# Kernel tuning notes

Hardware: AMD Instinct MI355X
Metric: run time of the kernel (lower is better)

Reference implementation:

```python
import jax, jax.numpy as jnp
import numpy as np

A_CONST = -50.0  # self.a in FNNnew


def _fnn_all(t, w1, b1, w2, b2):
    # Evaluate the 4 tiny FNNs (f, f_prime, g, g_prime) at once.
    # t: (L,); w1: (4,5,1); b1: (4,5); w2: (4,1,5); b2: (4,1) -> (4, L)
    z = jnp.tanh(jnp.einsum('l,kh->klh', t, w1[:, :, 0]) + b1[:, None, :])  # (4,L,5)
    out = jnp.einsum('klh,kh->kl', z, w2[:, 0, :]) + b2  # (4,L)
    return out * jnp.exp(A_CONST * t)[None, :]


def setup_inputs() -> dict:
    key = jax.random.key(0)
    ks = jax.random.split(key, 5)
    bs, d, T = 32, 8, 8192
    return {
        'x_data': jax.random.normal(ks[0], (bs, d, T), dtype=jnp.float32),
        'fnn_w1': jax.random.normal(ks[1], (4, 5, 1), dtype=jnp.float32) * 0.1,
        'fnn_b1': jax.random.normal(ks[2], (4, 5), dtype=jnp.float32) * 0.1,
        'fnn_w2': jax.random.normal(ks[3], (4, 1, 5), dtype=jnp.float32) * 0.1,
        'fnn_b2': jax.random.normal(ks[4], (4, 1), dtype=jnp.float32) * 0.1,
        'words': 8,
    }


def reference(x_data, fnn_w1, fnn_b1, fnn_w2, fnn_b2, words):
    bs, d, T = x_data.shape
    N = 3 * T + 1  # padded FFT length
    t = jnp.arange(T + 1, dtype=jnp.float32)

    arrs = _fnn_all(t, fnn_w1, fnn_b1, fnn_w2, fnn_b2)  # (4, T+1)
    f_arr = arrs[0][::-1]      # f, flipped
    fp_arr = arrs[1][::-1]     # f_prime, flipped
    g_arr = arrs[2]            # g
    gp_arr = arrs[3]           # g_prime

    pad1 = lambda a: jnp.pad(a, (T, T))  # (T+1,) -> (N,)
    Hf = jnp.fft.fft(pad1(f_arr))
    Hfp = jnp.fft.fft(pad1(fp_arr))
    Hg = jnp.fft.fft(pad1(g_arr))
    Hgp = jnp.fft.fft(pad1(gp_arr))
    Hones = jnp.fft.fft(pad1(jnp.ones(T + 1, jnp.float32)))

    # ISS low-rank arrays for all words at once (word k uses channels k%d, (k+1)%d)
    k = jnp.arange(words)
    dx1 = x_data[:, k % d, :]        # (bs, words, T)
    dx2 = x_data[:, (k + 1) % d, :]  # (bs, words, T)
    c1 = jnp.cumsum(dx1, -1)
    c2 = jnp.cumsum(dx2, -1)
    c1_prev = jnp.concatenate([jnp.zeros_like(c1[..., :1]), c1[..., :-1]], -1)
    pre0 = lambda a: jnp.concatenate([jnp.zeros_like(a[..., :1]), a], -1)  # -> length T+1
    iss_sum = pre0(jnp.cumsum(dx2 * c1_prev, -1))   # iterated sum <12>
    cs_d1 = pre0(c1)                                 # consecutive sum, level 1
    cs_d2 = pre0(c2)                                 # consecutive sum, level 2
    iss_d1 = pre0(jnp.cumsum(dx1 * dx2, -1))        # diagonal term

    pad3 = lambda a: jnp.pad(a, ((0, 0), (0, 0), (T, T)))
    F = lambda a: jnp.fft.fft(pad3(a), axis=-1)  # (bs, words, N) complex
    ISSf, C1f, C2f, D1f = F(iss_sum), F(cs_d1), F(cs_d2), F(iss_d1)

    conv = lambda Ha, Hb: jnp.fft.ifft(Ha * Hb, axis=-1)

    AA = conv(Hf, ISSf)
    AB = jnp.fft.ifft(Hg * Hones)       # (N,)
    BA = conv(Hfp, ISSf)
    BB = jnp.fft.ifft(Hgp * Hones)
    CA = conv(Hf, C1f)
    CB = conv(Hg, C2f)
    DA = conv(Hfp, C1f)
    DB = conv(Hgp, C2f)
    EA = jnp.fft.ifft(Hf * Hones)       # (N,)
    EB = conv(Hg, D1f)
    FA = jnp.fft.ifft(Hfp * Hones)      # (N,)
    FB = conv(Hgp, D1f)

    out = 0.5 * (AA * AB[None, None, :] + BA * BB[None, None, :]
                 + CA * CB + DA * DB
                 + EA[None, None, :] * EB + FA[None, None, :] * FB)
    return out.real[..., 2 * T:]  # (bs, words, T+1)
```

## Files before the change

kernel.cpp:

```cpp
#include <hip/hip_runtime.h>


constexpr int T  = 8192;
constexpr int BS = 32;
constexpr int D  = 8;
constexpr int W  = 8;
constexpr int L  = 3;

__global__ __launch_bounds__(256)
void pdn_kernel(const float* __restrict__ x,
                const float* __restrict__ w1,
                const float* __restrict__ b1,
                const float* __restrict__ w2,
                const float* __restrict__ b2,
                float* __restrict__ out)
{
    const int row = blockIdx.x;
    const int bb  = row >> 3;
    const int wd  = row & 7;
    const int tid = threadIdx.x;
    const float* dx1 = x + ((size_t)bb * D + wd) * T;
    const float* dx2 = x + ((size_t)bb * D + ((wd + 1) & 7)) * T;
    const size_t base = (size_t)row * (T + 1);
    float* orow = out + base;

    float s2 = 0.f, p = 0.f;
    const float4* v1 = (const float4*)dx1;
    const float4* v2 = (const float4*)dx2;
    #pragma unroll 4
    for (int t = tid; t < T / 4; t += 256) {
        float4 a = v1[t], c = v2[t];
        s2 += (c.x + c.y) + (c.z + c.w);
        p  += a.x * c.x + a.y * c.y + a.z * c.z + a.w * c.w;
    }

    const int align = (int)((4 - (base & 3)) & 3);
    if (tid < align) orow[tid] = 0.f;
    const int nvec = (T + 1 - align) >> 2;
    const int rem  = (T + 1 - align) - (nvec << 2);
    float4* ov = (float4*)(orow + align);
    const float4 z4 = make_float4(0.f, 0.f, 0.f, 0.f);
    #pragma unroll 4
    for (int i = tid; i < nvec; i += 256) ov[i] = z4;
    if (tid < rem) orow[align + (nvec << 2) + tid] = 0.f;

    for (int off = 32; off > 0; off >>= 1) {
        s2 += __shfl_down(s2, off);
        p  += __shfl_down(p,  off);
    }
    __shared__ float sh[2][4];
    __shared__ float term[4 * L * 5];
    const int wave = tid >> 6, lane = tid & 63;
    if (lane == 0) { sh[0][wave] = s2; sh[1][wave] = p; }

    if (tid < 4 * L * 5) {
        const int k = tid / (L * 5);
        const int r = tid % (L * 5);
        const int l = r / 5, h = r % 5;
        term[tid] = tanhf((float)l * w1[k * 5 + h] + b1[k * 5 + h]) * w2[k * 5 + h];
    }
    __syncthreads();

    if (tid != 0) return;

    const float s2tot = sh[0][0] + sh[0][1] + sh[0][2] + sh[0][3];
    const float ptot  = sh[1][0] + sh[1][1] + sh[1][2] + sh[1][3];

    const float e[L] = {1.0f, expf(-50.0f), expf(-100.0f)};
    float F[4][L];
    for (int k = 0; k < 4; ++k)
        for (int l = 0; l < L; ++l) {
            float acc = b2[k];
            for (int h = 0; h < 5; ++h) acc += term[(k * L + l) * 5 + h];
            F[k][l] = acc * e[l];
        }

    float S1[L], Q[L];
    S1[0] = 0.f; Q[0] = 0.f;
    for (int j = 1; j < L; ++j) {
        S1[j] = S1[j - 1] + dx1[j - 1];
        Q[j]  = Q[j - 1] + dx2[j - 1] * S1[j - 1];
    }
    float S2v[2 * L - 1], Pv[2 * L - 1];
    S2v[0] = s2tot; Pv[0] = ptot;
    for (int i = 1; i < 2 * L - 1; ++i) {
        S2v[i] = S2v[i - 1] - dx2[T - i];
        Pv[i]  = Pv[i - 1]  - dx1[T - i] * dx2[T - i];
    }
    float Gsum = 0.f, GPsum = 0.f;
    for (int l = 0; l < L; ++l) { Gsum += F[2][l]; GPsum += F[3][l]; }

    for (int m = 0; m < L; ++m) {
        float AA = 0, BA = 0, CA = 0, DA = 0, EA = 0, FA = 0;
        for (int l = m; l < L; ++l) {
            const float q = Q[l - m], s1 = S1[l - m];
            AA += F[0][l] * q;   BA += F[1][l] * q;
            CA += F[0][l] * s1;  DA += F[1][l] * s1;
            EA += F[0][l];       FA += F[1][l];
        }
        float CB = 0, DB = 0, EB = 0, FB = 0;
        for (int l = 0; l < L; ++l) {
            CB += F[2][l] * S2v[m + l]; DB += F[3][l] * S2v[m + l];
            EB += F[2][l] * Pv[m + l];  FB += F[3][l] * Pv[m + l];
        }
        orow[T - m] = 0.5f * (AA * Gsum + BA * GPsum + CA * CB + DA * DB + EA * EB + FA * FB);
    }
}

extern "C" void kernel_launch(void* const* d_in, const int* in_sizes, int n_in,
                              void* d_out, int out_size, void* d_ws, size_t ws_size,
                              hipStream_t stream)
{
    const float* x  = (const float*)d_in[0];
    const float* w1 = (const float*)d_in[1];
    const float* b1 = (const float*)d_in[2];
    const float* w2 = (const float*)d_in[3];
    const float* b2 = (const float*)d_in[4];
    float* out = (float*)d_out;

    pdn_kernel<<<BS * W, 256, 0, stream>>>(x, w1, b1, w2, b2, out);
}
```

Baseline: 10.14 us.

## Split row reduction and zero-fill across slices with separate epilogue kernel

Each output row's reduction and zero-fill is split across 8 blocks instead of one, so 2048 blocks launch instead of 256 and the GPU is better filled. Each block writes partial sums to workspace. A second small kernel combines the partials and computes the boundary outputs. This adds a second kernel launch and a round trip through global memory for the partials.

Result: slower. 12.76 us (+25.8%).

```diff
diff --git a/kernel.cpp b/kernel.cpp
--- a/kernel.cpp
+++ b/kernel.cpp
@@ -6,65 +6,94 @@
 constexpr int D  = 8;
 constexpr int W  = 8;
 constexpr int L  = 3;
+constexpr int SL = 8;
+constexpr int CH = T / SL;
 
 __global__ __launch_bounds__(256)
-void pdn_kernel(const float* __restrict__ x,
-                const float* __restrict__ w1,
-                const float* __restrict__ b1,
-                const float* __restrict__ w2,
-                const float* __restrict__ b2,
-                float* __restrict__ out)
+void pdn_reduce_fill(const float* __restrict__ x,
+                     float* __restrict__ out,
+                     float2* __restrict__ partials)
 {
-    const int row = blockIdx.x;
+    const int bid = blockIdx.x;
+    const int row = bid >> 3;
+    const int sl  = bid & 7;
     const int bb  = row >> 3;
     const int wd  = row & 7;
     const int tid = threadIdx.x;
-    const float* dx1 = x + ((size_t)bb * D + wd) * T;
-    const float* dx2 = x + ((size_t)bb * D + ((wd + 1) & 7)) * T;
-    const size_t base = (size_t)row * (T + 1);
-    float* orow = out + base;
 
-    float s2 = 0.f, p = 0.f;
-    const float4* v1 = (const float4*)dx1;
-    const float4* v2 = (const float4*)dx2;
-    #pragma unroll 4
-    for (int t = tid; t < T / 4; t += 256) {
-        float4 a = v1[t], c = v2[t];
-        s2 += (c.x + c.y) + (c.z + c.w);
-        p  += a.x * c.x + a.y * c.y + a.z * c.z + a.w * c.w;
-    }
+    const float* dx1 = x + ((size_t)bb * D + wd) * T + sl * CH;
+    const float* dx2 = x + ((size_t)bb * D + ((wd + 1) & 7)) * T + sl * CH;
 
+    const float4 a = ((const float4*)dx1)[tid];
+    const float4 c = ((const float4*)dx2)[tid];
+
+    const size_t base = (size_t)row * (T + 1) + (size_t)sl * CH;
+    float* o = out + base;
     const int align = (int)((4 - (base & 3)) & 3);
-    if (tid < align) orow[tid] = 0.f;
-    const int nvec = (T + 1 - align) >> 2;
-    const int rem  = (T + 1 - align) - (nvec << 2);
-    float4* ov = (float4*)(orow + align);
+    if (tid < align) o[tid] = 0.f;
+    const int nv  = (CH - align) >> 2;
+    const int rem = CH - align - (nv << 2);
+    float4* ov = (float4*)(o + align);
     const float4 z4 = make_float4(0.f, 0.f, 0.f, 0.f);
-    #pragma unroll 4
-    for (int i = tid; i < nvec; i += 256) ov[i] = z4;
-    if (tid < rem) orow[align + (nvec << 2) + tid] = 0.f;
+    if (tid < nv) ov[tid] = z4;
+    if (tid < rem) o[align + (nv << 2) + tid] = 0.f;
+    if (sl == SL - 1 && tid == 0) out[(size_t)row * (T + 1) + T] = 0.f;
 
+    float s2 = (c.x + c.y) + (c.z + c.w);
+    float p  = a.x * c.x + a.y * c.y + a.z * c.z + a.w * c.w;
     for (int off = 32; off > 0; off >>= 1) {
         s2 += __shfl_down(s2, off);
         p  += __shfl_down(p,  off);
     }
     __shared__ float sh[2][4];
-    __shared__ float term[4 * L * 5];
     const int wave = tid >> 6, lane = tid & 63;
     if (lane == 0) { sh[0][wave] = s2; sh[1][wave] = p; }
+    __syncthreads();
+    if (tid == 0) {
+        float s = sh[0][0] + sh[0][1] + sh[0][2] + sh[0][3];
+        float q = sh[1][0] + sh[1][1] + sh[1][2] + sh[1][3];
+        partials[bid] = make_float2(s, q);
+    }
+}
 
-    if (tid < 4 * L * 5) {
-        const int k = tid / (L * 5);
-        const int r = tid % (L * 5);
+__global__ __launch_bounds__(64)
+void pdn_epilogue(const float* __restrict__ x,
+                  const float* __restrict__ w1,
+                  const float* __restrict__ b1,
+                  const float* __restrict__ w2,
+                  const float* __restrict__ b2,
+                  const float2* __restrict__ partials,
+                  float* __restrict__ out)
+{
+    const int row  = blockIdx.x;
+    const int lane = threadIdx.x;
+    const int bb   = row >> 3;
+    const int wd   = row & 7;
+    const float* dx1 = x + ((size_t)bb * D + wd) * T;
+    const float* dx2 = x + ((size_t)bb * D + ((wd + 1) & 7)) * T;
+    float* orow = out + (size_t)row * (T + 1);
+
+    __shared__ float term[4 * L * 5];
+    if (lane < 4 * L * 5) {
+        const int k = lane / (L * 5);
+        const int r = lane % (L * 5);
         const int l = r / 5, h = r % 5;
-        term[tid] = tanhf((float)l * w1[k * 5 + h] + b1[k * 5 + h]) * w2[k * 5 + h];
+        term[lane] = tanhf((float)l * w1[k * 5 + h] + b1[k * 5 + h]) * w2[k * 5 + h];
+    }
+
+    float s2 = 0.f, p = 0.f;
+    if (lane < SL) {
+        const float2 t = partials[row * SL + lane];
+        s2 = t.x; p = t.y;
+    }
+    for (int off = SL / 2; off > 0; off >>= 1) {
+        s2 += __shfl_down(s2, off);
+        p  += __shfl_down(p,  off);
     }
     __syncthreads();
+    if (lane != 0) return;
 
-    if (tid != 0) return;
-
-    const float s2tot = sh[0][0] + sh[0][1] + sh[0][2] + sh[0][3];
-    const float ptot  = sh[1][0] + sh[1][1] + sh[1][2] + sh[1][3];
+    const float s2tot = s2, ptot = p;
 
     const float e[L] = {1.0f, expf(-50.0f), expf(-100.0f)};
     float F[4][L];
@@ -117,6 +146,8 @@
     const float* w2 = (const float*)d_in[3];
     const float* b2 = (const float*)d_in[4];
     float* out = (float*)d_out;
+    float2* partials = (float2*)d_ws;
 
-    pdn_kernel<<<BS * W, 256, 0, stream>>>(x, w1, b1, w2, b2, out);
+    pdn_reduce_fill<<<BS * W * SL, 256, 0, stream>>>(x, out, partials);
+    pdn_epilogue<<<BS * W, 64, 0, stream>>>(x, w1, b1, w2, b2, partials, out);
 }
```

## Split output zero-fill into separate blocks from reduction blocks

Applied to the files above, without the earlier changes.

Adds 2048 dedicated blocks that each zero one 1024-element slice of an output row. The original 256 blocks now only run the per-row reductions and write the three nonzero tail values. This removes the serial zero-fill loop from each reduction block and spreads store traffic over many more blocks, so the GPU's compute units stay busier. In exchange it adds extra block launches, and the slice sizes must line up exactly with the tail the reduction blocks write.

Result: no change. 9.959 us (-1.8%).

```diff
diff --git a/kernel.cpp b/kernel.cpp
--- a/kernel.cpp
+++ b/kernel.cpp
@@ -6,44 +6,53 @@
 constexpr int D  = 8;
 constexpr int W  = 8;
 constexpr int L  = 3;
+constexpr int NFILL = BS * W * 8;
+constexpr int CH = 1024;
 
 __global__ __launch_bounds__(256)
-void pdn_kernel(const float* __restrict__ x,
-                const float* __restrict__ w1,
-                const float* __restrict__ b1,
-                const float* __restrict__ w2,
-                const float* __restrict__ b2,
-                float* __restrict__ out)
+void pdn_fused(const float* __restrict__ x,
+               const float* __restrict__ w1,
+               const float* __restrict__ b1,
+               const float* __restrict__ w2,
+               const float* __restrict__ b2,
+               float* __restrict__ out)
 {
-    const int row = blockIdx.x;
+    const int bid = blockIdx.x;
+    const int tid = threadIdx.x;
+
+    if (bid < NFILL) {
+        const int row = bid >> 3;
+        const int sl  = bid & 7;
+        const size_t base = (size_t)row * (T + 1) + (size_t)sl * CH;
+        float* o = out + base;
+        const int n = (sl == 7) ? CH - 2 : CH;
+        const int align = (int)((4 - (base & 3)) & 3);
+        if (tid < align) o[tid] = 0.f;
+        const int nv  = (n - align) >> 2;
+        const int rem = n - align - (nv << 2);
+        float4* ov = (float4*)(o + align);
+        if (tid < nv) ov[tid] = make_float4(0.f, 0.f, 0.f, 0.f);
+        if (tid < rem) o[align + (nv << 2) + tid] = 0.f;
+        return;
+    }
+
+    const int row = bid - NFILL;
     const int bb  = row >> 3;
     const int wd  = row & 7;
-    const int tid = threadIdx.x;
     const float* dx1 = x + ((size_t)bb * D + wd) * T;
     const float* dx2 = x + ((size_t)bb * D + ((wd + 1) & 7)) * T;
-    const size_t base = (size_t)row * (T + 1);
-    float* orow = out + base;
+    float* orow = out + (size_t)row * (T + 1);
 
-    float s2 = 0.f, p = 0.f;
     const float4* v1 = (const float4*)dx1;
     const float4* v2 = (const float4*)dx2;
-    #pragma unroll 4
-    for (int t = tid; t < T / 4; t += 256) {
-        float4 a = v1[t], c = v2[t];
+    float s2 = 0.f, p = 0.f;
+    #pragma unroll
+    for (int i = 0; i < 8; ++i) {
+        const float4 a = v1[tid + 256 * i];
+        const float4 c = v2[tid + 256 * i];
         s2 += (c.x + c.y) + (c.z + c.w);
         p  += a.x * c.x + a.y * c.y + a.z * c.z + a.w * c.w;
     }
-
-    const int align = (int)((4 - (base & 3)) & 3);
-    if (tid < align) orow[tid] = 0.f;
-    const int nvec = (T + 1 - align) >> 2;
-    const int rem  = (T + 1 - align) - (nvec << 2);
-    float4* ov = (float4*)(orow + align);
-    const float4 z4 = make_float4(0.f, 0.f, 0.f, 0.f);
-    #pragma unroll 4
-    for (int i = tid; i < nvec; i += 256) ov[i] = z4;
-    if (tid < rem) orow[align + (nvec << 2) + tid] = 0.f;
-
     for (int off = 32; off > 0; off >>= 1) {
         s2 += __shfl_down(s2, off);
         p  += __shfl_down(p,  off);
@@ -60,7 +69,6 @@
         term[tid] = tanhf((float)l * w1[k * 5 + h] + b1[k * 5 + h]) * w2[k * 5 + h];
     }
     __syncthreads();
-
     if (tid != 0) return;
 
     const float s2tot = sh[0][0] + sh[0][1] + sh[0][2] + sh[0][3];
@@ -118,5 +126,5 @@
     const float* b2 = (const float*)d_in[4];
     float* out = (float*)d_out;
 
-    pdn_kernel<<<BS * W, 256, 0, stream>>>(x, w1, b1, w2, b2, out);
+    pdn_fused<<<NFILL + BS * W, 256, 0, stream>>>(x, w1, b1, w2, b2, out);
 }
```
